# Performance work log

Measured on AMD Instinct MI355X. Metric: run time of the kernel, lower is better.

The kernel has to match this reference:

```python
import jax, jax.numpy as jnp
import numpy as np
import math

B, S, D = 4, 2048, 1024
H, DK, DV = 16, 64, 64

def setup_inputs() -> dict:
    key = jax.random.key(0)
    ks = jax.random.split(key, 8)
    query = jax.random.normal(ks[0], (B, S, D), dtype=jnp.float32)
    key_t = jax.random.normal(ks[1], (B, S, D), dtype=jnp.float32)
    value = jax.random.normal(ks[2], (B, S, D), dtype=jnp.float32)
    # causal mask: True = masked (filled with -inf), broadcast over [B,H,S,S]
    mask = jnp.triu(jnp.ones((S, S), dtype=bool), k=1)[None, None, :, :]
    s = 0.02
    w_q = jax.random.normal(ks[3], (D, H * DK), dtype=jnp.float32) * s
    w_k = jax.random.normal(ks[4], (D, H * DK), dtype=jnp.float32) * s
    w_v = jax.random.normal(ks[5], (D, H * DV), dtype=jnp.float32) * s
    w_o = jax.random.normal(ks[6], (H * DV, D), dtype=jnp.float32) * s
    return {"query": query, "key": key_t, "value": value, "mask": mask,
            "w_q": w_q, "w_k": w_k, "w_v": w_v, "w_o": w_o}

def reference(query, key, value, mask, w_q, w_k, w_v, w_o):
    b, s, _ = query.shape
    # projections -> [B, H, S, dk/dv]
    q = (query @ w_q).reshape(b, s, H, DK).transpose(0, 2, 1, 3)
    k = (key @ w_k).reshape(b, s, H, DK).transpose(0, 2, 1, 3)
    v = (value @ w_v).reshape(b, s, H, DV).transpose(0, 2, 1, 3)
    scores = jnp.einsum('bhqd,bhkd->bhqk', q, k) / math.sqrt(DK)
    scores = jnp.where(mask, -jnp.inf, scores)
    attn = jax.nn.softmax(scores, axis=-1)
    out = jnp.einsum('bhqk,bhkd->bhqd', attn, v)
    out = out.transpose(0, 2, 1, 3).reshape(b, s, H * DV)
    return out @ w_o
```

## Files before the change

### kernel.cpp

```cpp
#include <hip/hip_runtime.h>
#include <hip/hip_bf16.h>

#define S_LEN 2048
#define NH 16
#define DHEAD 64
#define DMODEL 1024
#define BATCH 4

typedef __attribute__((ext_vector_type(4))) float f32x4;
typedef __attribute__((ext_vector_type(8))) short bf16x8;
typedef __attribute__((ext_vector_type(4))) short s16x4;
typedef __attribute__((ext_vector_type(4))) float fl4;
typedef __attribute__((ext_vector_type(4))) unsigned u32x4;
typedef __attribute__((ext_vector_type(2))) unsigned u32x2;

static __device__ __forceinline__ short f2bf(float f) {
  unsigned u = __builtin_bit_cast(unsigned, f);
  u += 0x7fffu + ((u >> 16) & 1u);
  return (short)(u >> 16);
}
static __device__ __forceinline__ f32x4 mfma16(bf16x8 a, bf16x8 b, f32x4 c) {
  return __builtin_amdgcn_mfma_f32_16x16x32_bf16(a, b, c, 0, 0, 0);
}
static __device__ __forceinline__ void gl_lds16(const short* g, short* l) {
  __builtin_amdgcn_global_load_lds(
      (const __attribute__((address_space(1))) unsigned*)g,
      (__attribute__((address_space(3))) unsigned*)l, 16, 0, 0);
}
static __device__ __forceinline__ unsigned cvt_pk_bf16(float lo, float hi) {
  unsigned r;
  asm("v_cvt_pk_bf16_f32 %0, %1, %2" : "=v"(r) : "v"(lo), "v"(hi));
  return r;
}

__global__ __launch_bounds__(256) void transpose_w3(
    const float* __restrict__ w0, const float* __restrict__ w1,
    const float* __restrict__ w2, short* __restrict__ o0,
    short* __restrict__ o1, short* __restrict__ o2) {
  const float* W = blockIdx.z == 0 ? w0 : blockIdx.z == 1 ? w1 : w2;
  short* O = blockIdx.z == 0 ? o0 : blockIdx.z == 1 ? o1 : o2;
  __shared__ __align__(16) short T[64][72];
  const int tid = threadIdx.x;
  const int k0 = blockIdx.y * 64, n0 = blockIdx.x * 64;
#pragma unroll
  for (int i = 0; i < 4; ++i) {
    int c = tid + i * 256;
    int kk = c >> 4, nn = (c & 15) << 2;
    fl4 v = *(const fl4*)(W + (size_t)(k0 + kk) * DMODEL + n0 + nn);
    T[nn + 0][kk] = f2bf(v.x);
    T[nn + 1][kk] = f2bf(v.y);
    T[nn + 2][kk] = f2bf(v.z);
    T[nn + 3][kk] = f2bf(v.w);
  }
  __syncthreads();
#pragma unroll
  for (int i = 0; i < 4; ++i) {
    int c = tid + i * 256;
    int nn = c >> 4, kk = (c & 15) << 2;
    *(s16x4*)(O + (size_t)(n0 + nn) * DMODEL + k0 + kk) = *(const s16x4*)&T[nn][kk];
  }
}

__global__ __launch_bounds__(256) void transpose_w1(
    const float* __restrict__ W, short* __restrict__ O) {
  __shared__ __align__(16) short T[64][72];
  const int tid = threadIdx.x;
  const int k0 = blockIdx.y * 64, n0 = blockIdx.x * 64;
#pragma unroll
  for (int i = 0; i < 4; ++i) {
    int c = tid + i * 256;
    int kk = c >> 4, nn = (c & 15) << 2;
    fl4 v = *(const fl4*)(W + (size_t)(k0 + kk) * DMODEL + n0 + nn);
    T[nn + 0][kk] = f2bf(v.x);
    T[nn + 1][kk] = f2bf(v.y);
    T[nn + 2][kk] = f2bf(v.z);
    T[nn + 3][kk] = f2bf(v.w);
  }
  __syncthreads();
#pragma unroll
  for (int i = 0; i < 4; ++i) {
    int c = tid + i * 256;
    int nn = c >> 4, kk = (c & 15) << 2;
    *(s16x4*)(O + (size_t)(n0 + nn) * DMODEL + k0 + kk) = *(const s16x4*)&T[nn][kk];
  }
}

template <int OUT_MODE, bool AF32>
__global__ __launch_bounds__(256) void gemm128(
    const float* __restrict__ Af, const short* __restrict__ Ab,
    const short* __restrict__ Bt, void* __restrict__ OutP, float scale) {
  __shared__ __align__(16) short As[128 * 64];
  __shared__ __align__(16) short Bs[128 * 64];
  const int tid = threadIdx.x, lane = tid & 63, wid = tid >> 6;
  const int m0 = blockIdx.x * 128, n0 = blockIdx.y * 128;
  const int wm = (wid >> 1) * 64, wn = (wid & 1) * 64;
  const int lr = lane & 15, g = lane >> 4;

  f32x4 acc[4][4] = {};

  const int baseRow = tid >> 3;
  const int colOff = (((tid & 7) ^ (baseRow & 7)) << 3);
  const int slot0 = g ^ (lr & 7);

  fl4 av[8];
  if (AF32) {
#pragma unroll
    for (int i = 0; i < 8; ++i) {
      const int c = tid + i * 256;
      av[i] = *(const fl4*)(Af + (size_t)(m0 + (c >> 4)) * DMODEL + ((c & 15) << 2));
    }
  }

  for (int k0 = 0; k0 < DMODEL; k0 += 64) {
    __syncthreads();
    if (AF32) {
#pragma unroll
      for (int i = 0; i < 8; ++i) {
        const int c = tid + i * 256;
        const int row = c >> 4, colc = c & 15;
        u32x2 pk;
        pk.x = cvt_pk_bf16(av[i].x, av[i].y);
        pk.y = cvt_pk_bf16(av[i].z, av[i].w);
        *(u32x2*)&As[row * 64 + (((colc >> 1) ^ (row & 7)) << 3) + ((colc & 1) << 2)] = pk;
      }
    } else {
#pragma unroll
      for (int i = 0; i < 4; ++i) {
        const short* ga = Ab + (size_t)(m0 + baseRow + i * 32) * DMODEL + k0 + colOff;
        gl_lds16(ga, As + (tid + i * 256) * 8);
      }
    }
#pragma unroll
    for (int i = 0; i < 4; ++i) {
      const short* gb = Bt + (size_t)(n0 + baseRow + i * 32) * DMODEL + k0 + colOff;
      gl_lds16(gb, Bs + (tid + i * 256) * 8);
    }
    __syncthreads();

    if (AF32 && k0 + 64 < DMODEL) {
#pragma unroll
      for (int i = 0; i < 8; ++i) {
        const int c = tid + i * 256;
        av[i] = *(const fl4*)(Af + (size_t)(m0 + (c >> 4)) * DMODEL + k0 + 64 + ((c & 15) << 2));
      }
    }

#pragma unroll
    for (int ks = 0; ks < 2; ++ks) {
      const int so = (slot0 ^ (ks << 2)) << 3;
      bf16x8 af[4], bfr[4];
#pragma unroll
      for (int t = 0; t < 4; ++t) {
        af[t] = *(const bf16x8*)&As[(wm + t * 16 + lr) * 64 + so];
        bfr[t] = *(const bf16x8*)&Bs[(wn + t * 16 + lr) * 64 + so];
      }
#pragma unroll
      for (int mi = 0; mi < 4; ++mi)
#pragma unroll
        for (int ni = 0; ni < 4; ++ni)
          acc[mi][ni] = mfma16(af[mi], bfr[ni], acc[mi][ni]);
    }
  }

  if (OUT_MODE == 0) {
    short* Out = (short*)OutP;
#pragma unroll
    for (int mi = 0; mi < 4; ++mi)
#pragma unroll
      for (int ni = 0; ni < 4; ++ni) {
        const int n = n0 + wn + ni * 16 + lr;
        const int h = n >> 6, d = n & 63;
#pragma unroll
        for (int r = 0; r < 4; ++r) {
          const int m = m0 + wm + mi * 16 + g * 4 + r;
          const int b = m >> 11, s = m & (S_LEN - 1);
          Out[(((size_t)b * NH + h) * S_LEN + s) * DHEAD + d] =
              f2bf(acc[mi][ni][r] * scale);
        }
      }
  } else if (OUT_MODE == 1) {
    short* Out = (short*)OutP;
#pragma unroll
    for (int mi = 0; mi < 4; ++mi) {
      const int mb = m0 + wm + mi * 16 + g * 4;
      const int b = mb >> 11, s = mb & (S_LEN - 1);
#pragma unroll
      for (int ni = 0; ni < 4; ++ni) {
        const int n = n0 + wn + ni * 16 + lr;
        const int h = n >> 6, d = n & 63;
        s16x4 pv;
        pv.x = f2bf(acc[mi][ni][0]);
        pv.y = f2bf(acc[mi][ni][1]);
        pv.z = f2bf(acc[mi][ni][2]);
        pv.w = f2bf(acc[mi][ni][3]);
        *(s16x4*)(Out + (((size_t)b * NH + h) * DHEAD + d) * S_LEN + s) = pv;
      }
    }
  } else {
    float* Out = (float*)OutP;
#pragma unroll
    for (int mi = 0; mi < 4; ++mi)
#pragma unroll
      for (int ni = 0; ni < 4; ++ni) {
        const int n = n0 + wn + ni * 16 + lr;
#pragma unroll
        for (int r = 0; r < 4; ++r) {
          const int m = m0 + wm + mi * 16 + g * 4 + r;
          Out[(size_t)m * DMODEL + n] = acc[mi][ni][r];
        }
      }
  }
}

static __device__ __forceinline__ void softmax_pf_static(
    f32x4 (&st)[4], bf16x8& pf0, bf16x8& pf1) {
#pragma unroll
  for (int nj = 0; nj < 4; ++nj)
#pragma unroll
    for (int r = 0; r < 4; ++r)
      st[nj][r] = exp2f(st[nj][r]);
  unsigned pw[2][4];
#pragma unroll
  for (int kc = 0; kc < 2; ++kc)
#pragma unroll
    for (int jj = 0; jj < 2; ++jj) {
      unsigned a = cvt_pk_bf16(st[2 * kc][2 * jj], st[2 * kc][2 * jj + 1]);
      unsigned bb = cvt_pk_bf16(st[2 * kc + 1][2 * jj], st[2 * kc + 1][2 * jj + 1]);
      asm("v_permlane32_swap_b32 %0, %1" : "+v"(a), "+v"(bb));
      asm("v_permlane16_swap_b32 %0, %1" : "+v"(a), "+v"(bb));
      pw[kc][jj] = a;
      pw[kc][jj + 2] = bb;
    }
  u32x4 w0 = {pw[0][0], pw[0][1], pw[0][2], pw[0][3]};
  u32x4 w1 = {pw[1][0], pw[1][1], pw[1][2], pw[1][3]};
  pf0 = __builtin_bit_cast(bf16x8, w0);
  pf1 = __builtin_bit_cast(bf16x8, w1);
}

static __device__ __forceinline__ void attn_epilogue(
    f32x4 (&ot)[4], float lsum, int b, int h, int qa, int g,
    short* __restrict__ AO) {
  const float inv = 1.f / lsum;
  short* dst = AO + ((size_t)b * S_LEN + qa) * DMODEL + h * DHEAD + (g << 2);
#pragma unroll
  for (int nd = 0; nd < 4; ++nd) {
    s16x4 pv;
    pv.x = f2bf(ot[nd][0] * inv);
    pv.y = f2bf(ot[nd][1] * inv);
    pv.z = f2bf(ot[nd][2] * inv);
    pv.w = f2bf(ot[nd][3] * inv);
    *(s16x4*)(dst + nd * 16) = pv;
  }
}

__global__ __launch_bounds__(256) void attn9(
    const short* __restrict__ Qp, const short* __restrict__ Kp,
    const short* __restrict__ VT, short* __restrict__ AO) {
  __shared__ __align__(16) short KV[2][8192];
  const int tid = threadIdx.x, lane = tid & 63, wid = tid >> 6;
  const int lr = lane & 15, g = lane >> 4;
  const int id = blockIdx.x;
  const int xcd = id & 7;
  const int bh = xcd * 8 + ((id >> 3) & 7);
  const int sg = 31 - (id >> 6);
  const int t = sg * 4 + wid;
  const short* Qb = Qp + (size_t)bh * S_LEN * DHEAD;
  const short* Kb = Kp + (size_t)bh * S_LEN * DHEAD;
  const short* Vb = VT + (size_t)bh * DHEAD * S_LEN;
  const int b = bh >> 4, h = bh & 15;

  const int NT = sg + 1;
  const int q0 = t << 4;
  const int qa = q0 + lr;

  const int row1 = tid >> 3;
  const int col1 = (tid & 7) ^ (row1 & 7);
  const int kOff1 = row1 * DHEAD + col1 * 8;
  const int vOff1 = row1 * S_LEN + col1 * 8;

#define STAGE9(bufi, kvv) do {                                      \
    const short* ks_ = Kb + (size_t)(kvv) * DHEAD + kOff1;          \
    gl_lds16(ks_,               &KV[bufi][0] + tid * 8);            \
    gl_lds16(ks_ + 32 * DHEAD,  &KV[bufi][2048] + tid * 8);         \
    const short* vs_ = Vb + (kvv) + vOff1;                          \
    gl_lds16(vs_,               &KV[bufi][4096] + tid * 8);         \
    gl_lds16(vs_ + 32 * S_LEN,  &KV[bufi][6144] + tid * 8);         \
  } while (0)

  const int slot0 = g ^ (lr & 7);
  const int fOff0 = lr * 64 + slot0 * 8;
  const int fOff1 = lr * 64 + (slot0 ^ 4) * 8;

  bf16x8 qf[2];
  qf[0] = *(const bf16x8*)(Qb + (size_t)qa * DHEAD + (g << 3));
  qf[1] = *(const bf16x8*)(Qb + (size_t)qa * DHEAD + 32 + (g << 3));

  bf16x8 ones;
#pragma unroll
  for (int i = 0; i < 8; ++i) ones[i] = (short)0x3F80;

  f32x4 ot[4] = {};
  f32x4 lacc = {};

  STAGE9(0, 0);

  for (int it = 0; it < NT; ++it) {
    const int kv0 = it << 6;
    const int cb = it & 1;
    if (it + 1 < NT) {
      STAGE9(cb ^ 1, kv0 + 64);
      asm volatile("s_waitcnt vmcnt(4)" ::: "memory");
    } else {
      asm volatile("s_waitcnt vmcnt(0)" ::: "memory");
    }
    __builtin_amdgcn_s_barrier();

    const short* kb = &KV[cb][0];
    const short* vb = &KV[cb][4096];

    f32x4 st[4] = {};
    __builtin_amdgcn_s_setprio(1);
#pragma unroll
    for (int nj = 0; nj < 4; ++nj) {
      bf16x8 k0 = *(const bf16x8*)(kb + fOff0 + nj * 1024);
      bf16x8 k1 = *(const bf16x8*)(kb + fOff1 + nj * 1024);
      st[nj] = mfma16(k0, qf[0], st[nj]);
      st[nj] = mfma16(k1, qf[1], st[nj]);
    }
    __builtin_amdgcn_s_setprio(0);
    if (it == NT - 1) {
#pragma unroll
      for (int nj = 0; nj < 4; ++nj)
#pragma unroll
        for (int r = 0; r < 4; ++r)
          if (kv0 + nj * 16 + (g << 2) + r > qa) st[nj][r] = -1e30f;
    }
    bf16x8 pf0, pf1;
    softmax_pf_static(st, pf0, pf1);
    __builtin_amdgcn_s_setprio(1);
    lacc = mfma16(ones, pf0, lacc);
    lacc = mfma16(ones, pf1, lacc);
#pragma unroll
    for (int nd = 0; nd < 4; ++nd) {
      bf16x8 v0 = *(const bf16x8*)(vb + fOff0 + nd * 1024);
      bf16x8 v1 = *(const bf16x8*)(vb + fOff1 + nd * 1024);
      ot[nd] = mfma16(v0, pf0, ot[nd]);
      ot[nd] = mfma16(v1, pf1, ot[nd]);
    }
    __builtin_amdgcn_s_setprio(0);
    __builtin_amdgcn_s_barrier();
  }
#undef STAGE9

  attn_epilogue(ot, lacc[0], b, h, qa, g, AO);
}

extern "C" void kernel_launch(void* const* d_in, const int* in_sizes, int n_in,
                              void* d_out, int out_size, void* d_ws, size_t ws_size,
                              hipStream_t stream) {
  const float* query = (const float*)d_in[0];
  const float* key   = (const float*)d_in[1];
  const float* value = (const float*)d_in[2];
  const float* w_q = (const float*)d_in[4];
  const float* w_k = (const float*)d_in[5];
  const float* w_v = (const float*)d_in[6];
  const float* w_o = (const float*)d_in[7];

  const size_t QKV = (size_t)BATCH * NH * S_LEN * DHEAD;
  short* Qp = (short*)d_ws;
  short* Kp = Qp + QKV;
  short* Vt = Kp + QKV;
  short* AO = Vt + QKV;
  short* Wto = Qp;
  short* Wtq = (short*)d_out;
  short* Wtk = Wtq + (size_t)DMODEL * DMODEL;
  short* Wtv = Wtk + (size_t)DMODEL * DMODEL;

  dim3 blk(256);
  dim3 gg((BATCH * S_LEN) / 128, DMODEL / 128);
  const float qscale = 0.125f * 1.4426950408889634f;

  transpose_w3<<<dim3(16, 16, 3), blk, 0, stream>>>(w_q, w_k, w_v, Wtq, Wtk, Wtv);
  gemm128<0, true><<<gg, blk, 0, stream>>>(query, nullptr, Wtq, Qp, qscale);
  gemm128<0, true><<<gg, blk, 0, stream>>>(key,   nullptr, Wtk, Kp, 1.0f);
  gemm128<1, true><<<gg, blk, 0, stream>>>(value, nullptr, Wtv, Vt, 1.0f);
  attn9<<<dim3(2048), blk, 0, stream>>>(Qp, Kp, Vt, AO);
  transpose_w1<<<dim3(16, 16), blk, 0, stream>>>(w_o, Wto);
  gemm128<2, false><<<gg, blk, 0, stream>>>(nullptr, AO, Wto, d_out, 1.0f);
}
```

Before: 187.2 us.

## Process two 16-row query tiles per wave in attention to reuse K/V fragments

```diff
diff --git a/kernel.cpp b/kernel.cpp
--- a/kernel.cpp
+++ b/kernel.cpp
@@ -253,7 +253,7 @@
   }
 }
 
-__global__ __launch_bounds__(256) void attn9(
+__global__ __launch_bounds__(256) void attn10(
     const short* __restrict__ Qp, const short* __restrict__ Kp,
     const short* __restrict__ VT, short* __restrict__ AO) {
   __shared__ __align__(16) short KV[2][8192];
@@ -262,23 +262,24 @@
   const int id = blockIdx.x;
   const int xcd = id & 7;
   const int bh = xcd * 8 + ((id >> 3) & 7);
-  const int sg = 31 - (id >> 6);
-  const int t = sg * 4 + wid;
+  const int bx = 15 - (id >> 6);
+  const int t = bx * 4 + wid;
   const short* Qb = Qp + (size_t)bh * S_LEN * DHEAD;
   const short* Kb = Kp + (size_t)bh * S_LEN * DHEAD;
   const short* Vb = VT + (size_t)bh * DHEAD * S_LEN;
   const int b = bh >> 4, h = bh & 15;
 
-  const int NT = sg + 1;
-  const int q0 = t << 4;
-  const int qa = q0 + lr;
+  const int NTw = (t + 2) >> 1;
+  const int NTblk = 2 * bx + 2;
+  const int q0 = t << 5;
+  const int qaA = q0 + lr, qaB = q0 + 16 + lr;
 
   const int row1 = tid >> 3;
   const int col1 = (tid & 7) ^ (row1 & 7);
   const int kOff1 = row1 * DHEAD + col1 * 8;
   const int vOff1 = row1 * S_LEN + col1 * 8;
 
-#define STAGE9(bufi, kvv) do {                                      \
+#define STAGE10(bufi, kvv) do {                                     \
     const short* ks_ = Kb + (size_t)(kvv) * DHEAD + kOff1;          \
     gl_lds16(ks_,               &KV[bufi][0] + tid * 8);            \
     gl_lds16(ks_ + 32 * DHEAD,  &KV[bufi][2048] + tid * 8);         \
@@ -291,68 +292,83 @@
   const int fOff0 = lr * 64 + slot0 * 8;
   const int fOff1 = lr * 64 + (slot0 ^ 4) * 8;
 
-  bf16x8 qf[2];
-  qf[0] = *(const bf16x8*)(Qb + (size_t)qa * DHEAD + (g << 3));
-  qf[1] = *(const bf16x8*)(Qb + (size_t)qa * DHEAD + 32 + (g << 3));
+  bf16x8 qfA[2], qfB[2];
+  qfA[0] = *(const bf16x8*)(Qb + (size_t)qaA * DHEAD + (g << 3));
+  qfA[1] = *(const bf16x8*)(Qb + (size_t)qaA * DHEAD + 32 + (g << 3));
+  qfB[0] = *(const bf16x8*)(Qb + (size_t)qaB * DHEAD + (g << 3));
+  qfB[1] = *(const bf16x8*)(Qb + (size_t)qaB * DHEAD + 32 + (g << 3));
 
   bf16x8 ones;
 #pragma unroll
   for (int i = 0; i < 8; ++i) ones[i] = (short)0x3F80;
 
-  f32x4 ot[4] = {};
-  f32x4 lacc = {};
-
-  STAGE9(0, 0);
-
-  for (int it = 0; it < NT; ++it) {
+  f32x4 otA[4] = {}, otB[4] = {};
+  f32x4 laccA = {}, laccB = {};
+
+  STAGE10(0, 0);
+
+  for (int it = 0; it < NTblk; ++it) {
     const int kv0 = it << 6;
     const int cb = it & 1;
-    if (it + 1 < NT) {
-      STAGE9(cb ^ 1, kv0 + 64);
+    if (it + 1 < NTblk) {
+      STAGE10(cb ^ 1, kv0 + 64);
       asm volatile("s_waitcnt vmcnt(4)" ::: "memory");
     } else {
       asm volatile("s_waitcnt vmcnt(0)" ::: "memory");
     }
     __builtin_amdgcn_s_barrier();
 
-    const short* kb = &KV[cb][0];
-    const short* vb = &KV[cb][4096];
-
-    f32x4 st[4] = {};
-    __builtin_amdgcn_s_setprio(1);
-#pragma unroll
-    for (int nj = 0; nj < 4; ++nj) {
-      bf16x8 k0 = *(const bf16x8*)(kb + fOff0 + nj * 1024);
-      bf16x8 k1 = *(const bf16x8*)(kb + fOff1 + nj * 1024);
-      st[nj] = mfma16(k0, qf[0], st[nj]);
-      st[nj] = mfma16(k1, qf[1], st[nj]);
-    }
-    __builtin_amdgcn_s_setprio(0);
-    if (it == NT - 1) {
-#pragma unroll
-      for (int nj = 0; nj < 4; ++nj)
-#pragma unroll
-        for (int r = 0; r < 4; ++r)
-          if (kv0 + nj * 16 + (g << 2) + r > qa) st[nj][r] = -1e30f;
-    }
-    bf16x8 pf0, pf1;
-    softmax_pf_static(st, pf0, pf1);
-    __builtin_amdgcn_s_setprio(1);
-    lacc = mfma16(ones, pf0, lacc);
-    lacc = mfma16(ones, pf1, lacc);
-#pragma unroll
-    for (int nd = 0; nd < 4; ++nd) {
-      bf16x8 v0 = *(const bf16x8*)(vb + fOff0 + nd * 1024);
-      bf16x8 v1 = *(const bf16x8*)(vb + fOff1 + nd * 1024);
-      ot[nd] = mfma16(v0, pf0, ot[nd]);
-      ot[nd] = mfma16(v1, pf1, ot[nd]);
-    }
-    __builtin_amdgcn_s_setprio(0);
+    if (it < NTw) {
+      const short* kb = &KV[cb][0];
+      const short* vb = &KV[cb][4096];
+
+      f32x4 stA[4] = {}, stB[4] = {};
+      __builtin_amdgcn_s_setprio(1);
+#pragma unroll
+      for (int nj = 0; nj < 4; ++nj) {
+        bf16x8 k0 = *(const bf16x8*)(kb + fOff0 + nj * 1024);
+        bf16x8 k1 = *(const bf16x8*)(kb + fOff1 + nj * 1024);
+        stA[nj] = mfma16(k0, qfA[0], stA[nj]);
+        stA[nj] = mfma16(k1, qfA[1], stA[nj]);
+        stB[nj] = mfma16(k0, qfB[0], stB[nj]);
+        stB[nj] = mfma16(k1, qfB[1], stB[nj]);
+      }
+      __builtin_amdgcn_s_setprio(0);
+      if (it == NTw - 1) {
+#pragma unroll
+        for (int nj = 0; nj < 4; ++nj)
+#pragma unroll
+          for (int r = 0; r < 4; ++r) {
+            const int kv = kv0 + nj * 16 + (g << 2) + r;
+            if (kv > qaA) stA[nj][r] = -1e30f;
+            if (kv > qaB) stB[nj][r] = -1e30f;
+          }
+      }
+      bf16x8 pfA0, pfA1, pfB0, pfB1;
+      softmax_pf_static(stA, pfA0, pfA1);
+      softmax_pf_static(stB, pfB0, pfB1);
+      __builtin_amdgcn_s_setprio(1);
+      laccA = mfma16(ones, pfA0, laccA);
+      laccA = mfma16(ones, pfA1, laccA);
+      laccB = mfma16(ones, pfB0, laccB);
+      laccB = mfma16(ones, pfB1, laccB);
+#pragma unroll
+      for (int nd = 0; nd < 4; ++nd) {
+        bf16x8 v0 = *(const bf16x8*)(vb + fOff0 + nd * 1024);
+        bf16x8 v1 = *(const bf16x8*)(vb + fOff1 + nd * 1024);
+        otA[nd] = mfma16(v0, pfA0, otA[nd]);
+        otA[nd] = mfma16(v1, pfA1, otA[nd]);
+        otB[nd] = mfma16(v0, pfB0, otB[nd]);
+        otB[nd] = mfma16(v1, pfB1, otB[nd]);
+      }
+      __builtin_amdgcn_s_setprio(0);
+    }
     __builtin_amdgcn_s_barrier();
   }
-#undef STAGE9
-
-  attn_epilogue(ot, lacc[0], b, h, qa, g, AO);
+#undef STAGE10
+
+  attn_epilogue(otA, laccA[0], b, h, qaA, g, AO);
+  attn_epilogue(otB, laccB[0], b, h, qaB, g, AO);
 }
 
 extern "C" void kernel_launch(void* const* d_in, const int* in_sizes, int n_in,
@@ -384,7 +400,7 @@
   gemm128<0, true><<<gg, blk, 0, stream>>>(query, nullptr, Wtq, Qp, qscale);
   gemm128<0, true><<<gg, blk, 0, stream>>>(key,   nullptr, Wtk, Kp, 1.0f);
   gemm128<1, true><<<gg, blk, 0, stream>>>(value, nullptr, Wtv, Vt, 1.0f);
-  attn9<<<dim3(2048), blk, 0, stream>>>(Qp, Kp, Vt, AO);
+  attn10<<<dim3(1024), blk, 0, stream>>>(Qp, Kp, Vt, AO);
   transpose_w1<<<dim3(16, 16), blk, 0, stream>>>(w_o, Wto);
   gemm128<2, false><<<gg, blk, 0, stream>>>(nullptr, AO, Wto, d_out, 1.0f);
 }
```

After: 189.2 us. About the same (+1.0%).
